# Kernel optimization log

Measured on AMD Instinct MI355X. Metric: run time of the kernel, lower is better.

Reference implementation:

```python
import math
import jax, jax.numpy as jnp
import numpy as np

N, T, D, H, DH = 4, 2048, 1024, 16, 64
CAP = 30.0
EPS = 1e-5


def _layernorm(x, g, b):
    m = jnp.mean(x, axis=-1, keepdims=True)
    v = jnp.mean(jnp.square(x - m), axis=-1, keepdims=True)
    return (x - m) * jax.lax.rsqrt(v + EPS) * g + b


def _rope(x):
    # x: [N, H, t, d]; interleaved rotary (rotary-embedding-torch style), theta=10000
    t, d = x.shape[2], x.shape[3]
    inv_freq = 1.0 / (10000.0 ** (jnp.arange(0, d, 2, dtype=jnp.float32) / d))
    ang = jnp.arange(t, dtype=jnp.float32)[:, None] * inv_freq[None, :]  # [t, d/2]
    cos, sin = jnp.cos(ang), jnp.sin(ang)
    x1, x2 = x[..., 0::2], x[..., 1::2]
    r1 = x1 * cos - x2 * sin
    r2 = x1 * sin + x2 * cos
    return jnp.stack([r1, r2], axis=-1).reshape(x.shape)


def setup_inputs() -> dict:
    key = jax.random.key(0)
    ks = jax.random.split(key, 8)
    s = 0.02
    lengths = jax.random.randint(ks[6], (N,), T // 2, T + 1).astype(jnp.int32)
    key_padding_mask = jnp.arange(T)[None, :] >= lengths[:, None]  # True = pad
    attn_mask = jnp.triu(jnp.ones((T, T), dtype=bool), 1)  # causal: True = masked
    return {
        "x": jax.random.normal(ks[0], (N, T, D), jnp.float32),
        "ln_g": jnp.ones((D,), jnp.float32),
        "ln_b": jnp.zeros((D,), jnp.float32),
        "Wq": jax.random.normal(ks[1], (D, H * DH), jnp.float32) * s,
        "bq": jnp.zeros((H * DH,), jnp.float32),
        "Wk": jax.random.normal(ks[2], (D, H * DH), jnp.float32) * s,
        "bk": jnp.zeros((H * DH,), jnp.float32),
        "Wv": jax.random.normal(ks[3], (D, H * DH), jnp.float32) * s,
        "bv": jnp.zeros((H * DH,), jnp.float32),
        "Wo": jax.random.normal(ks[4], (H * DH, D), jnp.float32) * s,
        "bo": jnp.zeros((D,), jnp.float32),
        "key_padding_mask": key_padding_mask,
        "attn_mask": attn_mask,
        "key_value_sequence_lengths": lengths,
    }


def reference(x, ln_g, ln_b, Wq, bq, Wk, bk, Wv, bv, Wo, bo,
              key_padding_mask, attn_mask, key_value_sequence_lengths):
    n, t, _ = x.shape
    h = _layernorm(x, ln_g, ln_b)  # shared LN for q/k/v (self-attention)
    q = (h @ Wq + bq).reshape(n, t, H, DH).transpose(0, 2, 1, 3)  # [n,H,t,d]
    k = (h @ Wk + bk).reshape(n, t, H, DH).transpose(0, 2, 1, 3)
    v = (h @ Wv + bv).reshape(n, t, H, DH).transpose(0, 2, 1, 3)
    q = _rope(q)
    k = _rope(k)
    scores = jnp.einsum('bhtd,bhTd->bhtT', q, k) / math.sqrt(DH)
    scores = CAP * jnp.tanh(scores / CAP)  # tanh soft-cap
    mask = key_padding_mask[:, None, None, :] | attn_mask[None, None, :, :]
    scores = jnp.where(mask, -jnp.inf, scores)
    attn = jax.nn.softmax(scores, axis=-1)
    out = jnp.einsum('bhtT,bhTd->bhtd', attn, v)
    out = out.transpose(0, 2, 1, 3).reshape(n, t, H * DH)
    return out @ Wo + bo
```

## Files before the change

### kernel.cpp

```cpp
#include <hip/hip_runtime.h>
#include <hip/hip_bf16.h>

typedef unsigned short u16;
typedef unsigned int   u32;
typedef __bf16 bf16x8 __attribute__((ext_vector_type(8)));
typedef float  f32x4  __attribute__((ext_vector_type(4)));

#define NB 4
#define T_ 2048
#define D_ 1024
#define H_ 16
#define DH 64
#define M_ (NB * T_)
#define PSTR 72

__device__ __forceinline__ float bf2f(u16 u) {
    union { u32 i; float f; } v; v.i = ((u32)u) << 16; return v.f;
}
__device__ __forceinline__ u16 f2bf(float f) {
    __bf16 b = (__bf16)f;
    union { __bf16 b; u16 u; } v; v.b = b; return v.u;
}

__device__ __forceinline__ void gl_lds16(const u16* g, u16* l) {
    __builtin_amdgcn_global_load_lds((const __attribute__((address_space(1))) void*)g,
                                     (__attribute__((address_space(3))) void*)l,
                                     16, 0, 0);
}

__device__ __forceinline__ int detect_f32(const u16* p) {
    int weird = 0;
    const int lane = threadIdx.x & 63;
    #pragma unroll
    for (int i = 0; i < 4; ++i) {
        const u16 u = p[lane * 4 + i];
        const int e = (u >> 7) & 0xFF;
        weird += (e == 0xFF || (e >= 0x01 && e <= 0x3F) || (e >= 0xC0 && e <= 0xFE));
    }
    #pragma unroll
    for (int off = 32; off; off >>= 1) weird += __shfl_xor(weird, off);
    return weird >= 16;
}

__device__ __forceinline__ int read_len(const void* raw, int b) {
    const int* a32 = (const int*)raw;
    bool ok32 = true;
    #pragma unroll
    for (int i = 0; i < NB; ++i) {
        const int v = a32[i];
        if (v < 1 || v > T_) ok32 = false;
    }
    int v = ok32 ? a32[b] : (int)((const long long*)raw)[b];
    return min(max(v, 1), T_);
}

__global__ __launch_bounds__(256) void ln_kernel(const void* __restrict__ xraw,
                                                 const void* __restrict__ graw,
                                                 const void* __restrict__ braw,
                                                 u16* __restrict__ h) {
    const int row = blockIdx.x;
    const int tid = threadIdx.x;
    const int isf = detect_f32((const u16*)xraw);

    float xv[4];
    if (isf) {
        const float* xr = (const float*)xraw + (size_t)row * D_;
        *(float4*)xv = *(const float4*)&xr[tid * 4];
    } else {
        const u16* xr = (const u16*)xraw + (size_t)row * D_;
        u16 loc[4] __attribute__((aligned(8)));
        *(uint2*)loc = *(const uint2*)&xr[tid * 4];
        #pragma unroll
        for (int i = 0; i < 4; ++i) xv[i] = bf2f(loc[i]);
    }

    float s = xv[0] + xv[1] + xv[2] + xv[3];
    float q = xv[0]*xv[0] + xv[1]*xv[1] + xv[2]*xv[2] + xv[3]*xv[3];

    #pragma unroll
    for (int off = 32; off; off >>= 1) {
        s += __shfl_xor(s, off);
        q += __shfl_xor(q, off);
    }
    __shared__ float red[8];
    const int wave = tid >> 6, lane = tid & 63;
    if (lane == 0) { red[wave] = s; red[4 + wave] = q; }
    __syncthreads();
    s = red[0] + red[1] + red[2] + red[3];
    q = red[4] + red[5] + red[6] + red[7];

    const float mean = s * (1.0f / D_);
    const float var  = q * (1.0f / D_) - mean * mean;
    const float rs   = rsqrtf(var + 1e-5f);

    u16 o[4] __attribute__((aligned(8)));
    #pragma unroll
    for (int i = 0; i < 4; ++i) {
        const int c = tid * 4 + i;
        const float gv = isf ? ((const float*)graw)[c] : bf2f(((const u16*)graw)[c]);
        const float bv = isf ? ((const float*)braw)[c] : bf2f(((const u16*)braw)[c]);
        o[i] = f2bf((xv[i] - mean) * rs * gv + bv);
    }
    *(uint2*)&h[(size_t)row * D_ + tid * 4] = *(uint2*)o;
}

__global__ __launch_bounds__(256) void wconv_kernel(const void* __restrict__ Wraw,
                                                    u16* __restrict__ Wt) {
    __shared__ u16 tile[64][PSTR];
    const int isf = detect_f32((const u16*)Wraw);
    const int n0 = blockIdx.x * 64;
    const int k0 = blockIdx.y * 64;
    const int tid = threadIdx.x;
    const int tr  = tid >> 2;
    const int tc  = (tid & 3) * 16;

    if (isf) {
        const float* W = (const float*)Wraw;
        #pragma unroll
        for (int i = 0; i < 16; ++i)
            tile[tc + i][tr] = f2bf(W[(size_t)(k0 + tr) * D_ + n0 + tc + i]);
    } else {
        const u16* W = (const u16*)Wraw;
        #pragma unroll
        for (int i = 0; i < 16; ++i)
            tile[tc + i][tr] = W[(size_t)(k0 + tr) * D_ + n0 + tc + i];
    }
    __syncthreads();
    *(uint4*)&Wt[(size_t)(n0 + tr) * D_ + k0 + tc]     = *(uint4*)&tile[tr][tc];
    *(uint4*)&Wt[(size_t)(n0 + tr) * D_ + k0 + tc + 8] = *(uint4*)&tile[tr][tc + 8];
}

__global__ __launch_bounds__(256) void rope_kernel(float2* __restrict__ tab) {
    const int gid = blockIdx.x * 256 + threadIdx.x;
    const int t = gid >> 5, i = gid & 31;
    const float inv = exp2f(-(float)i * 0.41524101186092f);
    const float ang = (float)t * inv;
    float sv, cv;
    sincosf(ang, &sv, &cv);
    tab[gid] = make_float2(cv, sv);
}

__global__ __launch_bounds__(256) void vtrans_kernel(const u16* __restrict__ vtmp,
                                                     u16* __restrict__ vt) {
    __shared__ u16 tile[64][PSTR];
    const int bh = blockIdx.y;
    const int b  = bh >> 4;
    const int hh = bh & 15;
    const int t0 = blockIdx.x * 64;
    const int tid = threadIdx.x;
    const int tr  = tid >> 2;
    const int tc  = (tid & 3) * 16;

    #pragma unroll
    for (int i = 0; i < 16; ++i)
        tile[tc + i][tr] = vtmp[(size_t)(b * T_ + t0 + tr) * D_ + hh * DH + tc + i];
    __syncthreads();
    u16* dst = vt + (size_t)bh * DH * T_ + (size_t)tr * T_ + t0;
    *(uint4*)&dst[tc]     = *(uint4*)&tile[tr][tc];
    *(uint4*)&dst[tc + 8] = *(uint4*)&tile[tr][tc + 8];
}

__global__ __launch_bounds__(256) void qkv_kernel(const u16* __restrict__ A,
                                                  const u16* __restrict__ Wt3,
                                                  const void* __restrict__ Braw,
                                                  const void* __restrict__ bqr,
                                                  const void* __restrict__ bkr,
                                                  const void* __restrict__ bvr,
                                                  u16* __restrict__ qo,
                                                  u16* __restrict__ ko,
                                                  u16* __restrict__ vo,
                                                  const float2* __restrict__ tab) {
    __shared__ __align__(16) u16 As[128 * 32];
    __shared__ __align__(16) u16 Bs[128 * 32];

    const int tid   = threadIdx.x;
    const int wave  = tid >> 6;
    const int lane  = tid & 63;
    const int quad  = lane >> 4;
    const int lr    = lane & 15;
    const int ntile = blockIdx.x * 128;
    const int mtile = blockIdx.y * 128;
    const int seg   = ntile >> 10;

    const int isf = detect_f32((const u16*)Braw);

    const int srow = wave * 32 + (lane >> 2);
    const int scol = (lane & 3) * 8;
    const u16* aptr0 = A   + (size_t)(mtile + srow) * D_ + scol;
    const u16* aptr1 = A   + (size_t)(mtile + srow + 16) * D_ + scol;
    const u16* bptr0 = Wt3 + (size_t)(ntile + srow) * D_ + scol;
    const u16* bptr1 = Wt3 + (size_t)(ntile + srow + 16) * D_ + scol;
    u16* alds0 = As + wave * 1024;
    u16* alds1 = As + wave * 1024 + 512;
    u16* blds0 = Bs + wave * 1024;
    u16* blds1 = Bs + wave * 1024 + 512;

    const int mbase = (wave >> 1) * 64;
    const int nbase = (wave & 1) * 64;

    f32x4 acc[4][4];
    #pragma unroll
    for (int m = 0; m < 4; ++m)
        #pragma unroll
        for (int n = 0; n < 4; ++n)
            acc[m][n] = (f32x4){0.f, 0.f, 0.f, 0.f};

    for (int k0 = 0; k0 < D_; k0 += 32) {
        gl_lds16(aptr0 + k0, alds0);
        gl_lds16(aptr1 + k0, alds1);
        gl_lds16(bptr0 + k0, blds0);
        gl_lds16(bptr1 + k0, blds1);
        __syncthreads();

        bf16x8 af[4], bfr[4];
        #pragma unroll
        for (int m = 0; m < 4; ++m)
            af[m] = *(const bf16x8*)&As[(mbase + m * 16 + lr) * 32 + quad * 8];
        #pragma unroll
        for (int n = 0; n < 4; ++n)
            bfr[n] = *(const bf16x8*)&Bs[(nbase + n * 16 + lr) * 32 + quad * 8];
        #pragma unroll
        for (int m = 0; m < 4; ++m)
            #pragma unroll
            for (int n = 0; n < 4; ++n)
                acc[m][n] = __builtin_amdgcn_mfma_f32_16x16x32_bf16(af[m], bfr[n], acc[m][n], 0, 0, 0);

        __syncthreads();
    }

    const void* biasraw = (seg == 0) ? bqr : (seg == 1) ? bkr : bvr;
    u16* out            = (seg == 0) ? qo  : (seg == 1) ? ko  : vo;
    const int nloc = (ntile & 1023) + nbase;

    #pragma unroll
    for (int m = 0; m < 4; ++m) {
        #pragma unroll
        for (int n = 0; n < 4; ++n) {
            const int ncl = nloc + n * 16 + lr;
            const float bv = isf ? ((const float*)biasraw)[ncl]
                                 : bf2f(((const u16*)biasraw)[ncl]);
            #pragma unroll
            for (int r = 0; r < 4; ++r) {
                const int mrow = mtile + mbase + m * 16 + quad * 4 + r;
                float v = acc[m][n][r] + bv;
                if (seg < 2) {
                    const float other = __shfl_xor(v, 1);
                    const int d = ncl & (DH - 1);
                    const int t = mrow & (T_ - 1);
                    const float2 cs = tab[t * 32 + (d >> 1)];
                    v = (d & 1) ? (other * cs.y + v * cs.x) : (v * cs.x - other * cs.y);
                }
                out[(size_t)mrow * D_ + ncl] = f2bf(v);
            }
        }
    }
}

__global__ __launch_bounds__(256) void gemm128_kernel(const u16* __restrict__ A,
                                                      const u16* __restrict__ Bt,
                                                      const void* __restrict__ Braw,
                                                      const void* __restrict__ biasraw,
                                                      void* __restrict__ out,
                                                      const int mode) {
    __shared__ __align__(16) u16 As[128 * 32];
    __shared__ __align__(16) u16 Bs[128 * 32];

    const int tid   = threadIdx.x;
    const int wave  = tid >> 6;
    const int lane  = tid & 63;
    const int quad  = lane >> 4;
    const int lr    = lane & 15;
    const int ntile = blockIdx.x * 128;
    const int mtile = blockIdx.y * 128;

    const int isf = detect_f32((const u16*)Braw);

    const int srow = wave * 32 + (lane >> 2);
    const int scol = (lane & 3) * 8;
    const u16* aptr0 = A  + (size_t)(mtile + srow) * D_ + scol;
    const u16* aptr1 = A  + (size_t)(mtile + srow + 16) * D_ + scol;
    const u16* bptr0 = Bt + (size_t)(ntile + srow) * D_ + scol;
    const u16* bptr1 = Bt + (size_t)(ntile + srow + 16) * D_ + scol;
    u16* alds0 = As + wave * 1024;
    u16* alds1 = As + wave * 1024 + 512;
    u16* blds0 = Bs + wave * 1024;
    u16* blds1 = Bs + wave * 1024 + 512;

    const int mbase = (wave >> 1) * 64;
    const int nbase = (wave & 1) * 64;

    f32x4 acc[4][4];
    #pragma unroll
    for (int m = 0; m < 4; ++m)
        #pragma unroll
        for (int n = 0; n < 4; ++n)
            acc[m][n] = (f32x4){0.f, 0.f, 0.f, 0.f};

    for (int k0 = 0; k0 < D_; k0 += 32) {
        gl_lds16(aptr0 + k0, alds0);
        gl_lds16(aptr1 + k0, alds1);
        gl_lds16(bptr0 + k0, blds0);
        gl_lds16(bptr1 + k0, blds1);
        __syncthreads();

        bf16x8 af[4], bfr[4];
        #pragma unroll
        for (int m = 0; m < 4; ++m)
            af[m] = *(const bf16x8*)&As[(mbase + m * 16 + lr) * 32 + quad * 8];
        #pragma unroll
        for (int n = 0; n < 4; ++n)
            bfr[n] = *(const bf16x8*)&Bs[(nbase + n * 16 + lr) * 32 + quad * 8];
        #pragma unroll
        for (int m = 0; m < 4; ++m)
            #pragma unroll
            for (int n = 0; n < 4; ++n)
                acc[m][n] = __builtin_amdgcn_mfma_f32_16x16x32_bf16(af[m], bfr[n], acc[m][n], 0, 0, 0);

        __syncthreads();
    }

    #pragma unroll
    for (int m = 0; m < 4; ++m) {
        #pragma unroll
        for (int n = 0; n < 4; ++n) {
            const int ncol = ntile + nbase + n * 16 + lr;
            const float bv = isf ? ((const float*)biasraw)[ncol]
                                 : bf2f(((const u16*)biasraw)[ncol]);
            #pragma unroll
            for (int r = 0; r < 4; ++r) {
                const int mrow = mtile + mbase + m * 16 + quad * 4 + r;
                float v = acc[m][n][r] + bv;
                if (mode == 2) {
                    const float other = __shfl_xor(v, 1);
                    const int d = ncol & (DH - 1);
                    const int t = mrow & (T_ - 1);
                    const int i = d >> 1;
                    const float inv = exp2f(-(float)i * 0.41524101186092f);
                    const float ang = (float)t * inv;
                    float sv, cv;
                    __sincosf(ang, &sv, &cv);
                    v = (d & 1) ? (other * sv + v * cv) : (v * cv - other * sv);
                }
                const int d  = ncol & (DH - 1);
                const int hh = ncol >> 6;
                const int t  = mrow & (T_ - 1);
                const int bb = mrow >> 11;
                if (mode == 0) {
                    if (isf) ((float*)out)[(size_t)mrow * D_ + ncol] = v;
                    else     ((u16*)out)[(size_t)mrow * D_ + ncol] = f2bf(v);
                } else if (mode == 1) {
                    ((u16*)out)[(((size_t)(bb * H_ + hh) * DH) + d) * T_ + t] = f2bf(v);
                } else {
                    ((u16*)out)[(((size_t)(bb * H_ + hh) * T_) + t) * DH + d] = f2bf(v);
                }
            }
        }
    }
}

__global__ __launch_bounds__(256) void gemm_kernel(const u16* __restrict__ A,
                                                   const void* __restrict__ Braw,
                                                   const void* __restrict__ biasraw,
                                                   void* __restrict__ out,
                                                   const int mode) {
    __shared__ __align__(16) u16 As[128 * 32];
    __shared__ __align__(16) u16 Bs[64 * 32];

    const int tid   = threadIdx.x;
    const int ntile = blockIdx.x * 64;
    const int mtile = blockIdx.y * 128;
    const int wave  = tid >> 6;
    const int lane  = tid & 63;
    const int quad  = lane >> 4;
    const int lr    = lane & 15;

    const int isf = detect_f32((const u16*)Braw);
    const float* Bf = (const float*)Braw;
    const u16*   Bu = (const u16*)Braw;

    f32x4 acc[2][4];
    #pragma unroll
    for (int s = 0; s < 2; ++s)
        #pragma unroll
        for (int n = 0; n < 4; ++n)
            acc[s][n] = (f32x4){0.f, 0.f, 0.f, 0.f};

    const int ar  = tid >> 1;
    const int akb = (tid & 1) * 16;
    const int bn  = tid & 63;
    const int bkb = (tid >> 6) * 8;
    const u16* Arow = A + (size_t)(mtile + ar) * D_ + akb;
    const size_t bcol0 = (size_t)bkb * D_ + ntile + bn;

    for (int k0 = 0; k0 < D_; k0 += 32) {
        *(uint4*)&As[ar * 32 + akb]     = *(const uint4*)(Arow + k0);
        *(uint4*)&As[ar * 32 + akb + 8] = *(const uint4*)(Arow + k0 + 8);
        {
            u16 tmp[8] __attribute__((aligned(16)));
            if (isf) {
                #pragma unroll
                for (int j = 0; j < 8; ++j) tmp[j] = f2bf(Bf[bcol0 + (size_t)(k0 + j) * D_]);
            } else {
                #pragma unroll
                for (int j = 0; j < 8; ++j) tmp[j] = Bu[bcol0 + (size_t)(k0 + j) * D_];
            }
            *(uint4*)&Bs[bn * 32 + bkb] = *(uint4*)tmp;
        }
        __syncthreads();

        const int mbase = wave * 32;
        bf16x8 af0 = *(const bf16x8*)&As[(mbase +      lr) * 32 + quad * 8];
        bf16x8 af1 = *(const bf16x8*)&As[(mbase + 16 + lr) * 32 + quad * 8];
        #pragma unroll
        for (int nt = 0; nt < 4; ++nt) {
            bf16x8 bf = *(const bf16x8*)&Bs[(nt * 16 + lr) * 32 + quad * 8];
            acc[0][nt] = __builtin_amdgcn_mfma_f32_16x16x32_bf16(af0, bf, acc[0][nt], 0, 0, 0);
            acc[1][nt] = __builtin_amdgcn_mfma_f32_16x16x32_bf16(af1, bf, acc[1][nt], 0, 0, 0);
        }
        __syncthreads();
    }

    #pragma unroll
    for (int s2 = 0; s2 < 2; ++s2) {
        #pragma unroll
        for (int nt = 0; nt < 4; ++nt) {
            const int ncol = ntile + nt * 16 + lr;
            const float bv = isf ? ((const float*)biasraw)[ncol]
                                 : bf2f(((const u16*)biasraw)[ncol]);
            #pragma unroll
            for (int r = 0; r < 4; ++r) {
                const int mrow = mtile + wave * 32 + s2 * 16 + quad * 4 + r;
                float v = acc[s2][nt][r] + bv;
                if (mode == 2) {
                    const float other = __shfl_xor(v, 1);
                    const int d = ncol & (DH - 1);
                    const int t = mrow & (T_ - 1);
                    const int i = d >> 1;
                    const float inv = exp2f(-(float)i * 0.41524101186092f);
                    const float ang = (float)t * inv;
                    const float cv = cosf(ang), sv = sinf(ang);
                    v = (d & 1) ? (other * sv + v * cv) : (v * cv - other * sv);
                }
                const int d  = ncol & (DH - 1);
                const int hh = ncol >> 6;
                const int t  = mrow & (T_ - 1);
                const int bb = mrow >> 11;
                if (mode == 0) {
                    if (isf) ((float*)out)[(size_t)mrow * D_ + ncol] = v;
                    else     ((u16*)out)[(size_t)mrow * D_ + ncol] = f2bf(v);
                } else if (mode == 1) {
                    ((u16*)out)[(((size_t)(bb * H_ + hh) * DH) + d) * T_ + t] = f2bf(v);
                } else {
                    ((u16*)out)[(((size_t)(bb * H_ + hh) * T_) + t) * DH + d] = f2bf(v);
                }
            }
        }
    }
}

__global__ __launch_bounds__(256) void attn_kernel(const u16* __restrict__ Q,
                                                   const u16* __restrict__ K,
                                                   const u16* __restrict__ Vt,
                                                   const void* __restrict__ lensraw,
                                                   u16* __restrict__ ctx,
                                                   const int rowmajor) {
    __shared__ __align__(16) u16 Ps[64 * PSTR];
    __shared__ __align__(16) u16 Ks[2][64 * PSTR];
    __shared__ __align__(16) u16 Vts[2][64 * PSTR];

    const int tid  = threadIdx.x;
    const int wave = tid >> 6;
    const int lane = tid & 63;
    const int quad = lane >> 4;
    const int lr   = lane & 15;
    const int bh   = blockIdx.y;
    const int qs   = blockIdx.x * 64;
    const int b    = bh >> 4;
    const int hh   = bh & 15;
    const int len  = read_len(lensraw, b);

    const size_t qkstride = rowmajor ? (size_t)D_ : (size_t)DH;
    const size_t qkoff    = rowmajor ? ((size_t)b * T_ * D_ + hh * DH)
                                     : ((size_t)bh * T_ * DH);
    const u16* Qp = Q + qkoff;
    const u16* Kp = K + qkoff;
    const u16* Vb = Vt + (size_t)bh * DH * T_;

    const int srow = tid >> 2;
    const int scb  = (tid & 3) * 16;

    *(uint4*)&Ps[srow * PSTR + scb]     = *(const uint4*)&Qp[(size_t)(qs + srow) * qkstride + scb];
    *(uint4*)&Ps[srow * PSTR + scb + 8] = *(const uint4*)&Qp[(size_t)(qs + srow) * qkstride + scb + 8];
    {
        uint4 k0 = *(const uint4*)&Kp[(size_t)srow * qkstride + scb];
        uint4 k1 = *(const uint4*)&Kp[(size_t)srow * qkstride + scb + 8];
        uint4 v0 = *(const uint4*)&Vb[(size_t)srow * T_ + scb];
        uint4 v1 = *(const uint4*)&Vb[(size_t)srow * T_ + scb + 8];
        *(uint4*)&Ks[0][srow * PSTR + scb]      = k0;
        *(uint4*)&Ks[0][srow * PSTR + scb + 8]  = k1;
        *(uint4*)&Vts[0][srow * PSTR + scb]     = v0;
        *(uint4*)&Vts[0][srow * PSTR + scb + 8] = v1;
    }
    __syncthreads();
    const bf16x8 qa0 = *(const bf16x8*)&Ps[(wave * 16 + lr) * PSTR + quad * 8];
    const bf16x8 qa1 = *(const bf16x8*)&Ps[(wave * 16 + lr) * PSTR + 32 + quad * 8];

    f32x4 acc[4];
    float l_loc[4] = {0.f, 0.f, 0.f, 0.f};
    #pragma unroll
    for (int nt = 0; nt < 4; ++nt) acc[nt] = (f32x4){0.f, 0.f, 0.f, 0.f};

    const int smax = min(qs + 63, len - 1);
    const int ktn  = smax / 64 + 1;
    const int prow = wave * 16 + quad * 4;

    const float C1 = 1.44269504f / 120.0f;
    const float C2 = -60.0f * 1.44269504f;

    int buf = 0;
    uint4 kr0, kr1, vr0, vr1;
    for (int kt = 0; kt < ktn; ++kt) {
        const int ks = kt * 64;
        const bool havenext = (kt + 1 < ktn);

        if (havenext) {
            const int ns = ks + 64;
            kr0 = *(const uint4*)&Kp[(size_t)(ns + srow) * qkstride + scb];
            kr1 = *(const uint4*)&Kp[(size_t)(ns + srow) * qkstride + scb + 8];
            vr0 = *(const uint4*)&Vb[(size_t)srow * T_ + ns + scb];
            vr1 = *(const uint4*)&Vb[(size_t)srow * T_ + ns + scb + 8];
        }

        f32x4 s[4];
        #pragma unroll
        for (int nt = 0; nt < 4; ++nt) s[nt] = (f32x4){0.f, 0.f, 0.f, 0.f};
        __builtin_amdgcn_s_setprio(1);
        #pragma unroll
        for (int nt = 0; nt < 4; ++nt) {
            bf16x8 kb0 = *(const bf16x8*)&Ks[buf][(nt * 16 + lr) * PSTR + quad * 8];
            bf16x8 kb1 = *(const bf16x8*)&Ks[buf][(nt * 16 + lr) * PSTR + 32 + quad * 8];
            s[nt] = __builtin_amdgcn_mfma_f32_16x16x32_bf16(qa0, kb0, s[nt], 0, 0, 0);
            s[nt] = __builtin_amdgcn_mfma_f32_16x16x32_bf16(qa1, kb1, s[nt], 0, 0, 0);
        }
        __builtin_amdgcn_s_setprio(0);

        const bool need_mask = (ks == qs) || (ks + 63 >= len);
        if (!need_mask) {
            #pragma unroll
            for (int r = 0; r < 4; ++r) {
                #pragma unroll
                for (int nt = 0; nt < 4; ++nt) {
                    const float z = exp2f(s[nt][r] * C1);
                    const float p = exp2f(C2 * __builtin_amdgcn_rcpf(z + 1.0f));
                    l_loc[r] += p;
                    Ps[(prow + r) * PSTR + nt * 16 + lr] = f2bf(p);
                }
            }
        } else {
            #pragma unroll
            for (int r = 0; r < 4; ++r) {
                const int trow = qs + prow + r;
                #pragma unroll
                for (int nt = 0; nt < 4; ++nt) {
                    const float z = exp2f(s[nt][r] * C1);
                    float p = exp2f(C2 * __builtin_amdgcn_rcpf(z + 1.0f));
                    const int col = ks + nt * 16 + lr;
                    p = (col > trow || col >= len) ? 0.f : p;
                    l_loc[r] += p;
                    Ps[(prow + r) * PSTR + nt * 16 + lr] = f2bf(p);
                }
            }
        }

        bf16x8 pa0 = *(const bf16x8*)&Ps[(wave * 16 + lr) * PSTR + quad * 8];
        bf16x8 pa1 = *(const bf16x8*)&Ps[(wave * 16 + lr) * PSTR + 32 + quad * 8];
        __builtin_amdgcn_s_setprio(1);
        #pragma unroll
        for (int nt = 0; nt < 4; ++nt) {
            bf16x8 vb0 = *(const bf16x8*)&Vts[buf][(nt * 16 + lr) * PSTR + quad * 8];
            bf16x8 vb1 = *(const bf16x8*)&Vts[buf][(nt * 16 + lr) * PSTR + 32 + quad * 8];
            acc[nt] = __builtin_amdgcn_mfma_f32_16x16x32_bf16(pa0, vb0, acc[nt], 0, 0, 0);
            acc[nt] = __builtin_amdgcn_mfma_f32_16x16x32_bf16(pa1, vb1, acc[nt], 0, 0, 0);
        }
        __builtin_amdgcn_s_setprio(0);

        if (havenext) {
            *(uint4*)&Ks[buf ^ 1][srow * PSTR + scb]      = kr0;
            *(uint4*)&Ks[buf ^ 1][srow * PSTR + scb + 8]  = kr1;
            *(uint4*)&Vts[buf ^ 1][srow * PSTR + scb]     = vr0;
            *(uint4*)&Vts[buf ^ 1][srow * PSTR + scb + 8] = vr1;
        }
        __syncthreads();
        buf ^= 1;
    }

    #pragma unroll
    for (int r = 0; r < 4; ++r) {
        float l = l_loc[r];
        #pragma unroll
        for (int off = 1; off < 16; off <<= 1) l += __shfl_xor(l, off);
        const float invl = (l > 0.f) ? (1.0f / l) : 0.f;
        const int qrow = prow + r;
        #pragma unroll
        for (int nt = 0; nt < 4; ++nt) {
            ctx[(size_t)(b * T_ + qs + qrow) * D_ + hh * DH + nt * 16 + lr] =
                f2bf(acc[nt][r] * invl);
        }
    }
}

extern "C" void kernel_launch(void* const* d_in, const int* in_sizes, int n_in,
                              void* d_out, int out_size, void* d_ws, size_t ws_size,
                              hipStream_t stream) {
    u16* h = (u16*)d_ws;
    const size_t MD = (size_t)M_ * D_;
    const size_t WD = (size_t)D_ * D_;
    u16* q  = h + MD;
    u16* k  = q + MD;
    u16* vt = k + MD;
    const bool havewt  = ws_size >= (4 * MD + 4 * WD) * sizeof(u16);
    const bool havebig = ws_size >= (5 * MD + 4 * WD) * sizeof(u16)
                                    + (size_t)T_ * 32 * sizeof(float2);
    u16* wtq = havewt ? (vt + MD)  : nullptr;
    u16* wtk = havewt ? (wtq + WD) : nullptr;
    u16* wtv = havewt ? (wtk + WD) : nullptr;
    u16* wto = havewt ? (wtv + WD) : nullptr;
    u16* vtmp = havebig ? (wto + WD) : nullptr;
    float2* tab = havebig ? (float2*)(vtmp + MD) : nullptr;

    ln_kernel<<<M_, 256, 0, stream>>>(d_in[0], d_in[1], d_in[2], h);

    if (havebig) {
        dim3 wgrid(D_ / 64, D_ / 64);
        wconv_kernel<<<wgrid, 256, 0, stream>>>(d_in[3], wtq);
        wconv_kernel<<<wgrid, 256, 0, stream>>>(d_in[5], wtk);
        wconv_kernel<<<wgrid, 256, 0, stream>>>(d_in[7], wtv);
        wconv_kernel<<<wgrid, 256, 0, stream>>>(d_in[9], wto);
        rope_kernel<<<256, 256, 0, stream>>>(tab);

        qkv_kernel<<<dim3(3 * D_ / 128, M_ / 128), 256, 0, stream>>>(
            h, wtq, d_in[3], d_in[4], d_in[6], d_in[8], q, k, vtmp, tab);

        vtrans_kernel<<<dim3(T_ / 64, NB * H_), 256, 0, stream>>>(vtmp, vt);

        attn_kernel<<<dim3(T_ / 64, NB * H_), 256, 0, stream>>>(q, k, vt, d_in[13], h, 1);

        gemm128_kernel<<<dim3(D_ / 128, M_ / 128), 256, 0, stream>>>(
            h, wto, d_in[9], d_in[10], d_out, 0);
    } else if (havewt) {
        dim3 wgrid(D_ / 64, D_ / 64);
        wconv_kernel<<<wgrid, 256, 0, stream>>>(d_in[3], wtq);
        wconv_kernel<<<wgrid, 256, 0, stream>>>(d_in[5], wtk);
        wconv_kernel<<<wgrid, 256, 0, stream>>>(d_in[7], wtv);
        wconv_kernel<<<wgrid, 256, 0, stream>>>(d_in[9], wto);

        dim3 g128(D_ / 128, M_ / 128);
        gemm128_kernel<<<g128, 256, 0, stream>>>(h, wtq, d_in[3], d_in[4], q, 2);
        gemm128_kernel<<<g128, 256, 0, stream>>>(h, wtk, d_in[5], d_in[6], k, 2);
        gemm128_kernel<<<g128, 256, 0, stream>>>(h, wtv, d_in[7], d_in[8], vt, 1);

        attn_kernel<<<dim3(T_ / 64, NB * H_), 256, 0, stream>>>(q, k, vt, d_in[13], h, 0);

        gemm128_kernel<<<g128, 256, 0, stream>>>(h, wto, d_in[9], d_in[10], d_out, 0);
    } else {
        dim3 ggrid(D_ / 64, M_ / 128);
        gemm_kernel<<<ggrid, 256, 0, stream>>>(h, d_in[3], d_in[4], q, 2);
        gemm_kernel<<<ggrid, 256, 0, stream>>>(h, d_in[5], d_in[6], k, 2);
        gemm_kernel<<<ggrid, 256, 0, stream>>>(h, d_in[7], d_in[8], vt, 1);

        attn_kernel<<<dim3(T_ / 64, NB * H_), 256, 0, stream>>>(q, k, vt, d_in[13], h, 0);

        gemm_kernel<<<ggrid, 256, 0, stream>>>(h, d_in[9], d_in[10], d_out, 0);
    }
}
```

Measured before the change: 435.0 us.

## Merge weight conversions, single-buffer attention LDS, use raw exp2 and bit-trick bf16

Replaces the four per-weight conversion launches with one kernel using a z-dimension over the four weights, cutting launch overhead. In attention, K/V shared memory drops from double to single buffering with an extra barrier before refilling. The intent is lower LDS use and higher occupancy, at the cost of an extra sync per tile. It also switches exp2f to the hardware builtin and replaces the bf16 cast with a manual round-to-nearest-even bit trick, which drops NaN handling.

```diff
diff --git a/kernel.cpp b/kernel.cpp
--- a/kernel.cpp
+++ b/kernel.cpp
@@ -18,8 +18,9 @@
     union { u32 i; float f; } v; v.i = ((u32)u) << 16; return v.f;
 }
 __device__ __forceinline__ u16 f2bf(float f) {
-    __bf16 b = (__bf16)f;
-    union { __bf16 b; u16 u; } v; v.b = b; return v.u;
+    union { float fl; u32 i; } v; v.fl = f;
+    u32 r = v.i + 0x7fff + ((v.i >> 16) & 1);
+    return (u16)(r >> 16);
 }
 
 __device__ __forceinline__ void gl_lds16(const u16* g, u16* l) {
@@ -102,6 +103,41 @@
         o[i] = f2bf((xv[i] - mean) * rs * gv + bv);
     }
     *(uint2*)&h[(size_t)row * D_ + tid * 4] = *(uint2*)o;
+}
+
+__global__ __launch_bounds__(256) void wconv4_kernel(const void* __restrict__ W0,
+                                                     const void* __restrict__ W1,
+                                                     const void* __restrict__ W2,
+                                                     const void* __restrict__ W3,
+                                                     u16* __restrict__ Wt0,
+                                                     u16* __restrict__ Wt1,
+                                                     u16* __restrict__ Wt2,
+                                                     u16* __restrict__ Wt3) {
+    __shared__ u16 tile[64][PSTR];
+    const int z = blockIdx.z;
+    const void* Wraw = (z == 0) ? W0 : (z == 1) ? W1 : (z == 2) ? W2 : W3;
+    u16* Wt          = (z == 0) ? Wt0 : (z == 1) ? Wt1 : (z == 2) ? Wt2 : Wt3;
+    const int isf = detect_f32((const u16*)Wraw);
+    const int n0 = blockIdx.x * 64;
+    const int k0 = blockIdx.y * 64;
+    const int tid = threadIdx.x;
+    const int tr  = tid >> 2;
+    const int tc  = (tid & 3) * 16;
+
+    if (isf) {
+        const float* W = (const float*)Wraw;
+        #pragma unroll
+        for (int i = 0; i < 16; ++i)
+            tile[tc + i][tr] = f2bf(W[(size_t)(k0 + tr) * D_ + n0 + tc + i]);
+    } else {
+        const u16* W = (const u16*)Wraw;
+        #pragma unroll
+        for (int i = 0; i < 16; ++i)
+            tile[tc + i][tr] = W[(size_t)(k0 + tr) * D_ + n0 + tc + i];
+    }
+    __syncthreads();
+    *(uint4*)&Wt[(size_t)(n0 + tr) * D_ + k0 + tc]     = *(uint4*)&tile[tr][tc];
+    *(uint4*)&Wt[(size_t)(n0 + tr) * D_ + k0 + tc + 8] = *(uint4*)&tile[tr][tc + 8];
 }
 
 __global__ __launch_bounds__(256) void wconv_kernel(const void* __restrict__ Wraw,
@@ -465,8 +501,8 @@
                                                    u16* __restrict__ ctx,
                                                    const int rowmajor) {
     __shared__ __align__(16) u16 Ps[64 * PSTR];
-    __shared__ __align__(16) u16 Ks[2][64 * PSTR];
-    __shared__ __align__(16) u16 Vts[2][64 * PSTR];
+    __shared__ __align__(16) u16 Ks[64 * PSTR];
+    __shared__ __align__(16) u16 Vts[64 * PSTR];
 
     const int tid  = threadIdx.x;
     const int wave = tid >> 6;
@@ -496,10 +532,10 @@
         uint4 k1 = *(const uint4*)&Kp[(size_t)srow * qkstride + scb + 8];
         uint4 v0 = *(const uint4*)&Vb[(size_t)srow * T_ + scb];
         uint4 v1 = *(const uint4*)&Vb[(size_t)srow * T_ + scb + 8];
-        *(uint4*)&Ks[0][srow * PSTR + scb]      = k0;
-        *(uint4*)&Ks[0][srow * PSTR + scb + 8]  = k1;
-        *(uint4*)&Vts[0][srow * PSTR + scb]     = v0;
-        *(uint4*)&Vts[0][srow * PSTR + scb + 8] = v1;
+        *(uint4*)&Ks[srow * PSTR + scb]      = k0;
+        *(uint4*)&Ks[srow * PSTR + scb + 8]  = k1;
+        *(uint4*)&Vts[srow * PSTR + scb]     = v0;
+        *(uint4*)&Vts[srow * PSTR + scb + 8] = v1;
     }
     __syncthreads();
     const bf16x8 qa0 = *(const bf16x8*)&Ps[(wave * 16 + lr) * PSTR + quad * 8];
@@ -517,7 +553,6 @@
     const float C1 = 1.44269504f / 120.0f;
     const float C2 = -60.0f * 1.44269504f;
 
-    int buf = 0;
     uint4 kr0, kr1, vr0, vr1;
     for (int kt = 0; kt < ktn; ++kt) {
         const int ks = kt * 64;
@@ -537,8 +572,8 @@
         __builtin_amdgcn_s_setprio(1);
         #pragma unroll
         for (int nt = 0; nt < 4; ++nt) {
-            bf16x8 kb0 = *(const bf16x8*)&Ks[buf][(nt * 16 + lr) * PSTR + quad * 8];
-            bf16x8 kb1 = *(const bf16x8*)&Ks[buf][(nt * 16 + lr) * PSTR + 32 + quad * 8];
+            bf16x8 kb0 = *(const bf16x8*)&Ks[(nt * 16 + lr) * PSTR + quad * 8];
+            bf16x8 kb1 = *(const bf16x8*)&Ks[(nt * 16 + lr) * PSTR + 32 + quad * 8];
             s[nt] = __builtin_amdgcn_mfma_f32_16x16x32_bf16(qa0, kb0, s[nt], 0, 0, 0);
             s[nt] = __builtin_amdgcn_mfma_f32_16x16x32_bf16(qa1, kb1, s[nt], 0, 0, 0);
         }
@@ -550,8 +585,8 @@
             for (int r = 0; r < 4; ++r) {
                 #pragma unroll
                 for (int nt = 0; nt < 4; ++nt) {
-                    const float z = exp2f(s[nt][r] * C1);
-                    const float p = exp2f(C2 * __builtin_amdgcn_rcpf(z + 1.0f));
+                    const float z = __builtin_amdgcn_exp2f(s[nt][r] * C1);
+                    const float p = __builtin_amdgcn_exp2f(C2 * __builtin_amdgcn_rcpf(z + 1.0f));
                     l_loc[r] += p;
                     Ps[(prow + r) * PSTR + nt * 16 + lr] = f2bf(p);
                 }
@@ -562,8 +597,8 @@
                 const int trow = qs + prow + r;
                 #pragma unroll
                 for (int nt = 0; nt < 4; ++nt) {
-                    const float z = exp2f(s[nt][r] * C1);
-                    float p = exp2f(C2 * __builtin_amdgcn_rcpf(z + 1.0f));
+                    const float z = __builtin_amdgcn_exp2f(s[nt][r] * C1);
+                    float p = __builtin_amdgcn_exp2f(C2 * __builtin_amdgcn_rcpf(z + 1.0f));
                     const int col = ks + nt * 16 + lr;
                     p = (col > trow || col >= len) ? 0.f : p;
                     l_loc[r] += p;
@@ -577,21 +612,21 @@
         __builtin_amdgcn_s_setprio(1);
         #pragma unroll
         for (int nt = 0; nt < 4; ++nt) {
-            bf16x8 vb0 = *(const bf16x8*)&Vts[buf][(nt * 16 + lr) * PSTR + quad * 8];
-            bf16x8 vb1 = *(const bf16x8*)&Vts[buf][(nt * 16 + lr) * PSTR + 32 + quad * 8];
+            bf16x8 vb0 = *(const bf16x8*)&Vts[(nt * 16 + lr) * PSTR + quad * 8];
+            bf16x8 vb1 = *(const bf16x8*)&Vts[(nt * 16 + lr) * PSTR + 32 + quad * 8];
             acc[nt] = __builtin_amdgcn_mfma_f32_16x16x32_bf16(pa0, vb0, acc[nt], 0, 0, 0);
             acc[nt] = __builtin_amdgcn_mfma_f32_16x16x32_bf16(pa1, vb1, acc[nt], 0, 0, 0);
         }
         __builtin_amdgcn_s_setprio(0);
 
         if (havenext) {
-            *(uint4*)&Ks[buf ^ 1][srow * PSTR + scb]      = kr0;
-            *(uint4*)&Ks[buf ^ 1][srow * PSTR + scb + 8]  = kr1;
-            *(uint4*)&Vts[buf ^ 1][srow * PSTR + scb]     = vr0;
-            *(uint4*)&Vts[buf ^ 1][srow * PSTR + scb + 8] = vr1;
-        }
-        __syncthreads();
-        buf ^= 1;
+            __syncthreads();
+            *(uint4*)&Ks[srow * PSTR + scb]      = kr0;
+            *(uint4*)&Ks[srow * PSTR + scb + 8]  = kr1;
+            *(uint4*)&Vts[srow * PSTR + scb]     = vr0;
+            *(uint4*)&Vts[srow * PSTR + scb + 8] = vr1;
+            __syncthreads();
+        }
     }
 
     #pragma unroll
@@ -631,11 +666,8 @@
     ln_kernel<<<M_, 256, 0, stream>>>(d_in[0], d_in[1], d_in[2], h);
 
     if (havebig) {
-        dim3 wgrid(D_ / 64, D_ / 64);
-        wconv_kernel<<<wgrid, 256, 0, stream>>>(d_in[3], wtq);
-        wconv_kernel<<<wgrid, 256, 0, stream>>>(d_in[5], wtk);
-        wconv_kernel<<<wgrid, 256, 0, stream>>>(d_in[7], wtv);
-        wconv_kernel<<<wgrid, 256, 0, stream>>>(d_in[9], wto);
+        wconv4_kernel<<<dim3(D_ / 64, D_ / 64, 4), 256, 0, stream>>>(
+            d_in[3], d_in[5], d_in[7], d_in[9], wtq, wtk, wtv, wto);
         rope_kernel<<<256, 256, 0, stream>>>(tab);
 
         qkv_kernel<<<dim3(3 * D_ / 128, M_ / 128), 256, 0, stream>>>(
```

New measurement: 386.4 us. 11.2% less time.
